# Optimization experiments

Hardware: AMD Instinct MI355X
Metric: run time of the kernel (lower is better)

Reference implementation:

```python
import jax, jax.numpy as jnp
import numpy as np

TEMPERATURE = 0.07
EPS = 1e-8  # torch cosine_similarity clamps the norm product at eps


def setup_inputs() -> dict:
    key = jax.random.key(0)
    k1, k2 = jax.random.split(key)
    B, D = 8192, 256
    u = jax.random.normal(k1, (B, D), dtype=jnp.float32)
    v = jax.random.normal(k2, (B, D), dtype=jnp.float32)
    return {"u": u, "v": v}


def _cos_sim_matrix(a, b):
    # pairwise cosine similarity: (a . b) / max(|a||b|, eps)
    dots = a @ b.T                                   # [B, B]
    an = jnp.linalg.norm(a, axis=-1)                 # [B]
    bn = jnp.linalg.norm(b, axis=-1)                 # [B]
    denom = jnp.maximum(an[:, None] * bn[None, :], EPS)
    return dots / denom


def reference(u, v):
    B = u.shape[0]
    sim_uv = _cos_sim_matrix(u, v) / TEMPERATURE     # [B, B]
    sim_uu = _cos_sim_matrix(u, u) / TEMPERATURE     # [B, B]
    eye = jnp.eye(B, dtype=bool)
    pos_loss = jnp.diagonal(sim_uv)                  # [B]
    neg_inf = jnp.array(-jnp.inf, dtype=sim_uv.dtype)
    # off-diagonal entries of both matrices, concatenated per row (2B-2 valid each)
    negative_sim = jnp.concatenate(
        [jnp.where(eye, neg_inf, sim_uv), jnp.where(eye, neg_inf, sim_uu)], axis=1
    )                                                # [B, 2B]
    neg_loss = jax.nn.logsumexp(negative_sim, axis=-1)  # [B]
    return (-pos_loss + neg_loss).mean()
```

## Files before the change

kernel.cpp:

```cpp
#include <hip/hip_runtime.h>
#include <hip/hip_bf16.h>
#include <stdint.h>

#define NB 8192
#define ND 256
#define NW 16384
#define BM 128
#define BN 128
#define NSTRIP 4
#define STRIPW 4096
#define NTILES (STRIPW / BN)
#define SQRT_INVT 3.7796447f

typedef __bf16 bf16x8 __attribute__((ext_vector_type(8)));
typedef float floatx4 __attribute__((ext_vector_type(4)));

__device__ __forceinline__ void gload_lds16(const void* g, void* l) {
    __builtin_amdgcn_global_load_lds(
        (const __attribute__((address_space(1))) unsigned int*)g,
        (__attribute__((address_space(3))) unsigned int*)l,
        16, 0, 0);
}

__global__ __launch_bounds__(512) void prep_kernel(
    const float* __restrict__ u, const float* __restrict__ v,
    __hip_bfloat16* __restrict__ W)
{
    const int t    = threadIdx.x;
    const int row  = blockIdx.x * 8 + (t >> 6);
    const int lane = t & 63;
    const float* src = (row < NB) ? (v + (size_t)row * ND)
                                  : (u + (size_t)(row - NB) * ND);
    float4 x = ((const float4*)src)[lane];
    float ss = x.x * x.x + x.y * x.y + x.z * x.z + x.w * x.w;
#pragma unroll
    for (int off = 1; off < 64; off <<= 1) ss += __shfl_xor(ss, off, 64);
    const float sc = rsqrtf(ss) * SQRT_INVT;
    ushort4 o;
    __hip_bfloat16 h;
    h = __float2bfloat16(x.x * sc); o.x = *(const unsigned short*)&h;
    h = __float2bfloat16(x.y * sc); o.y = *(const unsigned short*)&h;
    h = __float2bfloat16(x.z * sc); o.z = *(const unsigned short*)&h;
    h = __float2bfloat16(x.w * sc); o.w = *(const unsigned short*)&h;
    ((ushort4*)(W + (size_t)row * ND))[lane] = o;
}

__global__ __launch_bounds__(512, 2) void dcl_main(
    const __hip_bfloat16* __restrict__ W,
    float* __restrict__ partial,
    float* __restrict__ pos)
{
    const int b  = blockIdx.x;
    const int s  = (b >> 1) & 3;
    const int rt = ((b >> 3) << 1) | (b & 1);
    const int rb = rt * BM;

    const __hip_bfloat16* A = W + (size_t)NB * ND;

    __shared__ __align__(16) char lds[131072];

    const int tid  = threadIdx.x;
    const int wave = tid >> 6;
    const int lane = tid & 63;
    const int wm   = wave >> 2;
    const int wn   = wave & 3;
    const int quad = lane >> 4;
    const int tcol = lane & 15;

    {
        const int cb0 = s * STRIPW;
#pragma unroll
        for (int i = 0; i < 8; i++) {
            int o = i * 8192 + wave * 1024 + lane * 16;
            int r = o >> 9;
            int c = (o >> 4) & 31;
            int cg = (c ^ (r & 15)) * 8;
            gload_lds16(A + (size_t)(rb + r) * ND + cg,
                        lds + i * 8192 + wave * 1024);
            gload_lds16(W + (size_t)(cb0 + r) * ND + cg,
                        lds + 65536 + i * 8192 + wave * 1024);
        }
    }
    __syncthreads();

    bf16x8 af[4][8];
#pragma unroll
    for (int mt = 0; mt < 4; mt++) {
        int r = wm * 64 + mt * 16 + tcol;
#pragma unroll
        for (int ks = 0; ks < 8; ks++) {
            int c = (ks * 4 + quad) ^ (r & 15);
            af[mt][ks] = *(const bf16x8*)(lds + r * 512 + (c << 4));
        }
    }
    __syncthreads();

    float rsum[4][4];
#pragma unroll
    for (int mt = 0; mt < 4; mt++)
#pragma unroll
        for (int reg = 0; reg < 4; reg++) rsum[mt][reg] = 0.f;

    for (int ct = 0; ct < NTILES; ct++) {
        char* curB = (ct & 1) ? lds : (lds + 65536);
        if (ct + 1 < NTILES) {
            char* nxt = ((ct + 1) & 1) ? lds : (lds + 65536);
            const int cbn = s * STRIPW + (ct + 1) * BN;
#pragma unroll
            for (int i = 0; i < 8; i++) {
                int o = i * 8192 + wave * 1024 + lane * 16;
                int r = o >> 9;
                int c = (o >> 4) & 31;
                int cg = (c ^ (r & 15)) * 8;
                gload_lds16(W + (size_t)(cbn + r) * ND + cg,
                            nxt + i * 8192 + wave * 1024);
            }
        }
        const int cb = s * STRIPW + ct * BN;

        floatx4 acc[4][2];
#pragma unroll
        for (int mt = 0; mt < 4; mt++)
#pragma unroll
            for (int nt = 0; nt < 2; nt++) acc[mt][nt] = (floatx4){0.f, 0.f, 0.f, 0.f};

#pragma unroll
        for (int ks = 0; ks < 8; ks++) {
            bf16x8 bfr[2];
#pragma unroll
            for (int nt = 0; nt < 2; nt++) {
                int r = wn * 32 + nt * 16 + tcol;
                int c = (ks * 4 + quad) ^ (r & 15);
                bfr[nt] = *(const bf16x8*)(curB + r * 512 + (c << 4));
            }
#pragma unroll
            for (int mt = 0; mt < 4; mt++)
#pragma unroll
                for (int nt = 0; nt < 2; nt++)
                    acc[mt][nt] = __builtin_amdgcn_mfma_f32_16x16x32_bf16(
                        af[mt][ks], bfr[nt], acc[mt][nt], 0, 0, 0);
        }

        if (cb != rb && cb != rb + NB) {
#pragma unroll
            for (int mt = 0; mt < 4; mt++)
#pragma unroll
                for (int nt = 0; nt < 2; nt++)
#pragma unroll
                    for (int reg = 0; reg < 4; reg++)
                        rsum[mt][reg] += __expf(acc[mt][nt][reg]);
        } else {
            const bool isuv = (cb == rb);
#pragma unroll
            for (int mt = 0; mt < 4; mt++)
#pragma unroll
                for (int nt = 0; nt < 2; nt++) {
                    const int gcol = cb + wn * 32 + nt * 16 + tcol;
#pragma unroll
                    for (int reg = 0; reg < 4; reg++) {
                        const int grow = rb + wm * 64 + mt * 16 + quad * 4 + reg;
                        float sc = acc[mt][nt][reg];
                        bool diag = (gcol == grow + (isuv ? 0 : NB));
                        if (isuv && diag) pos[grow] = sc;
                        rsum[mt][reg] += diag ? 0.f : __expf(sc);
                    }
                }
        }
        __syncthreads();
    }

#pragma unroll
    for (int mt = 0; mt < 4; mt++)
#pragma unroll
        for (int reg = 0; reg < 4; reg++) {
            float vsum = rsum[mt][reg];
            vsum += __shfl_xor(vsum, 1, 64);
            vsum += __shfl_xor(vsum, 2, 64);
            vsum += __shfl_xor(vsum, 4, 64);
            vsum += __shfl_xor(vsum, 8, 64);
            if (tcol == 0) {
                int lrow = wm * 64 + mt * 16 + quad * 4 + reg;
                ((float*)lds)[wn * 128 + lrow] = vsum;
            }
        }
    __syncthreads();
    if (tid < BM) {
        const float* lf = (const float*)lds;
        float t = lf[tid] + lf[128 + tid] + lf[256 + tid] + lf[384 + tid];
        partial[(size_t)s * NB + rb + tid] = t;
    }
}

__global__ __launch_bounds__(1024) void finalize_kernel(
    const float* __restrict__ partial, const float* __restrict__ pos,
    float* __restrict__ out)
{
    const int t = threadIdx.x;
    float s = 0.f;
    for (int i = t; i < NB; i += 1024) {
        float tot = partial[i] + partial[NB + i] + partial[2 * NB + i]
                  + partial[3 * NB + i];
        s += logf(tot) - pos[i];
    }
#pragma unroll
    for (int off = 32; off > 0; off >>= 1) s += __shfl_down(s, off, 64);
    __shared__ float wsum[16];
    if ((t & 63) == 0) wsum[t >> 6] = s;
    __syncthreads();
    if (t == 0) {
        float tot = 0.f;
#pragma unroll
        for (int i = 0; i < 16; i++) tot += wsum[i];
        out[0] = tot / (float)NB;
    }
}

extern "C" void kernel_launch(void* const* d_in, const int* in_sizes, int n_in,
                              void* d_out, int out_size, void* d_ws, size_t ws_size,
                              hipStream_t stream) {
    const float* u = (const float*)d_in[0];
    const float* v = (const float*)d_in[1];
    float* out = (float*)d_out;

    char* ws = (char*)d_ws;
    __hip_bfloat16* W = (__hip_bfloat16*)ws;
    float* partial = (float*)(ws + (size_t)NW * ND * sizeof(__hip_bfloat16));
    float* pos     = partial + NSTRIP * NB;

    prep_kernel<<<NW / 8, 512, 0, stream>>>(u, v, W);
    dcl_main<<<256, 512, 0, stream>>>(W, partial, pos);
    finalize_kernel<<<1, 1024, 0, stream>>>(partial, pos, out);
}
```

Measured before the change: 135.3 us.

## Give each wave private double-buffered B tiles and software-pipeline exp with MFMA

Each wave now loads its own 16-row slice of the column tile into a private LDS double buffer. This removes the block-wide __syncthreads in the main loop and synchronises only with per-wave vmcnt waits. The loop is software-pipelined so the exp epilogue of one tile overlaps the MFMA of the next, with s_setprio raising priority around MFMA issue. Diagonal entries are handled by subtracting their exp after the fact rather than branching per tile. This trades smaller tiles (BN 64) and some exp-subtraction precision risk for less synchronisation and better overlap of the exp and MFMA work.

```diff
diff --git a/kernel.cpp b/kernel.cpp
--- a/kernel.cpp
+++ b/kernel.cpp
@@ -6,7 +6,7 @@
 #define ND 256
 #define NW 16384
 #define BM 128
-#define BN 128
+#define BN 64
 #define NSTRIP 4
 #define STRIPW 4096
 #define NTILES (STRIPW / BN)
@@ -66,20 +66,16 @@
     const int wn   = wave & 3;
     const int quad = lane >> 4;
     const int tcol = lane & 15;
-
-    {
-        const int cb0 = s * STRIPW;
-#pragma unroll
-        for (int i = 0; i < 8; i++) {
-            int o = i * 8192 + wave * 1024 + lane * 16;
-            int r = o >> 9;
-            int c = (o >> 4) & 31;
-            int cg = (c ^ (r & 15)) * 8;
-            gload_lds16(A + (size_t)(rb + r) * ND + cg,
-                        lds + i * 8192 + wave * 1024);
-            gload_lds16(W + (size_t)(cb0 + r) * ND + cg,
-                        lds + 65536 + i * 8192 + wave * 1024);
-        }
+    const int cc   = lane & 31;
+    const int rh   = lane >> 5;
+
+#pragma unroll
+    for (int i = 0; i < 8; i++) {
+        int o = i * 8192 + wave * 1024 + lane * 16;
+        int r = o >> 9;
+        int c = (o >> 4) & 31;
+        int cg = (c ^ (r & 15)) * 8;
+        gload_lds16(A + (size_t)(rb + r) * ND + cg, lds + i * 8192 + wave * 1024);
     }
     __syncthreads();
 
@@ -95,79 +91,106 @@
     }
     __syncthreads();
 
+    char* const wbuf  = lds + wave * 16384;
+    const int   sbase = s * STRIPW;
+
+    const bool isuv = (s < 2);
+    int dp = rb + wm * 64 + (isuv ? 0 : NB);
+    if ((dp >> 12) != s) dp = 0x40000000;
+
     float rsum[4][4];
 #pragma unroll
     for (int mt = 0; mt < 4; mt++)
 #pragma unroll
-        for (int reg = 0; reg < 4; reg++) rsum[mt][reg] = 0.f;
-
-    for (int ct = 0; ct < NTILES; ct++) {
-        char* curB = (ct & 1) ? lds : (lds + 65536);
-        if (ct + 1 < NTILES) {
-            char* nxt = ((ct + 1) & 1) ? lds : (lds + 65536);
-            const int cbn = s * STRIPW + (ct + 1) * BN;
-#pragma unroll
-            for (int i = 0; i < 8; i++) {
-                int o = i * 8192 + wave * 1024 + lane * 16;
-                int r = o >> 9;
-                int c = (o >> 4) & 31;
-                int cg = (c ^ (r & 15)) * 8;
-                gload_lds16(W + (size_t)(cbn + r) * ND + cg,
-                            nxt + i * 8192 + wave * 1024);
-            }
-        }
-        const int cb = s * STRIPW + ct * BN;
-
-        floatx4 acc[4][2];
-#pragma unroll
-        for (int mt = 0; mt < 4; mt++)
-#pragma unroll
-            for (int nt = 0; nt < 2; nt++) acc[mt][nt] = (floatx4){0.f, 0.f, 0.f, 0.f};
-
-#pragma unroll
-        for (int ks = 0; ks < 8; ks++) {
-            bf16x8 bfr[2];
-#pragma unroll
-            for (int nt = 0; nt < 2; nt++) {
-                int r = wn * 32 + nt * 16 + tcol;
-                int c = (ks * 4 + quad) ^ (r & 15);
-                bfr[nt] = *(const bf16x8*)(curB + r * 512 + (c << 4));
-            }
-#pragma unroll
-            for (int mt = 0; mt < 4; mt++)
-#pragma unroll
-                for (int nt = 0; nt < 2; nt++)
-                    acc[mt][nt] = __builtin_amdgcn_mfma_f32_16x16x32_bf16(
-                        af[mt][ks], bfr[nt], acc[mt][nt], 0, 0, 0);
-        }
-
-        if (cb != rb && cb != rb + NB) {
-#pragma unroll
-            for (int mt = 0; mt < 4; mt++)
-#pragma unroll
-                for (int nt = 0; nt < 2; nt++)
-#pragma unroll
-                    for (int reg = 0; reg < 4; reg++)
-                        rsum[mt][reg] += __expf(acc[mt][nt][reg]);
-        } else {
-            const bool isuv = (cb == rb);
-#pragma unroll
-            for (int mt = 0; mt < 4; mt++)
-#pragma unroll
-                for (int nt = 0; nt < 2; nt++) {
-                    const int gcol = cb + wn * 32 + nt * 16 + tcol;
-#pragma unroll
-                    for (int reg = 0; reg < 4; reg++) {
-                        const int grow = rb + wm * 64 + mt * 16 + quad * 4 + reg;
-                        float sc = acc[mt][nt][reg];
-                        bool diag = (gcol == grow + (isuv ? 0 : NB));
-                        if (isuv && diag) pos[grow] = sc;
-                        rsum[mt][reg] += diag ? 0.f : __expf(sc);
-                    }
-                }
-        }
-        __syncthreads();
-    }
+        for (int rg = 0; rg < 4; rg++) rsum[mt][rg] = 0.f;
+
+#define STAGE(t, half) do {                                                  \
+    const int rowb_ = sbase + (t) * BN + wn * 16;                            \
+    char* dst_ = wbuf + (half) * 8192;                                       \
+    _Pragma("unroll")                                                        \
+    for (int i_ = 0; i_ < 8; i_++) {                                         \
+        int r_ = 2 * i_ + rh;                                                \
+        gload_lds16(W + (size_t)(rowb_ + r_) * ND + ((cc ^ r_) << 3),        \
+                    dst_ + i_ * 1024);                                       \
+    }                                                                        \
+} while (0)
+
+#define EPI_CLEAN(accP) do {                                                 \
+    _Pragma("unroll")                                                        \
+    for (int mt_ = 0; mt_ < 4; mt_++)                                        \
+        _Pragma("unroll")                                                    \
+        for (int rg_ = 0; rg_ < 4; rg_++)                                    \
+            rsum[mt_][rg_] += __expf(accP[mt_][rg_]);                        \
+} while (0)
+
+#define FIXUP(accP, cbP) do {                                                \
+    if ((cbP) == dp) {                                                       \
+        _Pragma("unroll")                                                    \
+        for (int mt_ = 0; mt_ < 4; mt_++)                                    \
+            _Pragma("unroll")                                                \
+            for (int rg_ = 0; rg_ < 4; rg_++) {                              \
+                int rl_ = mt_ * 16 + quad * 4 + rg_;                         \
+                bool sel_ = (rl_ == wn * 16 + tcol);                         \
+                float sc_ = accP[mt_][rg_];                                  \
+                if (isuv && sel_) pos[rb + wm * 64 + rl_] = sc_;             \
+                if (sel_) rsum[mt_][rg_] -= __expf(sc_);                     \
+            }                                                                \
+    }                                                                        \
+} while (0)
+
+#define COMPUTE(acc, bufp) do {                                              \
+    _Pragma("unroll")                                                        \
+    for (int mt_ = 0; mt_ < 4; mt_++) acc[mt_] = (floatx4){0.f,0.f,0.f,0.f}; \
+    __builtin_amdgcn_s_setprio(1);                                           \
+    _Pragma("unroll")                                                        \
+    for (int ks_ = 0; ks_ < 8; ks_++) {                                      \
+        bf16x8 bb_ = *(const bf16x8*)((bufp) + tcol * 512 +                  \
+                                      ((((ks_ * 4) + quad) ^ tcol) << 4));   \
+        _Pragma("unroll")                                                    \
+        for (int mt_ = 0; mt_ < 4; mt_++)                                    \
+            acc[mt_] = __builtin_amdgcn_mfma_f32_16x16x32_bf16(              \
+                af[mt_][ks_], bb_, acc[mt_], 0, 0, 0);                       \
+    }                                                                        \
+    __builtin_amdgcn_s_setprio(0);                                           \
+} while (0)
+
+    floatx4 accA[4], accB[4];
+#pragma unroll
+    for (int mt = 0; mt < 4; mt++)
+        accB[mt] = (floatx4){-1e38f, -1e38f, -1e38f, -1e38f};
+    int cbA = -1, cbB = -1;
+
+    STAGE(0, 0);
+
+#pragma unroll 1
+    for (int t2 = 0; t2 < NTILES; t2 += 2) {
+        asm volatile("s_waitcnt vmcnt(0)" ::: "memory");
+        STAGE(t2 + 1, 1);
+        __builtin_amdgcn_sched_barrier(0);
+        EPI_CLEAN(accB);
+        COMPUTE(accA, wbuf);
+        __builtin_amdgcn_sched_barrier(0);
+        FIXUP(accB, cbB);
+        cbA = sbase + t2 * BN;
+
+        asm volatile("s_waitcnt vmcnt(0)" ::: "memory");
+        if (t2 + 2 < NTILES) STAGE(t2 + 2, 0);
+        __builtin_amdgcn_sched_barrier(0);
+        EPI_CLEAN(accA);
+        COMPUTE(accB, wbuf + 8192);
+        __builtin_amdgcn_sched_barrier(0);
+        FIXUP(accA, cbA);
+        cbB = sbase + (t2 + 1) * BN;
+    }
+    EPI_CLEAN(accB);
+    FIXUP(accB, cbB);
+
+#undef STAGE
+#undef EPI_CLEAN
+#undef FIXUP
+#undef COMPUTE
+
+    __syncthreads();
 
 #pragma unroll
     for (int mt = 0; mt < 4; mt++)
```

Result: no change. 137.4 us (+1.5%).

## Split column range into eight shards with 64-wide tiles and higher occupancy

Applied to the files above, without the earlier changes.

The work is split into 8 column shards of 2048 (512 blocks) instead of 4 strips (256 blocks). Tiles are now 64 columns wide, so LDS use halves to 64KB and launch bounds allow 4 blocks per CU. A fragments are now loaded directly from global into registers instead of staged through LDS. The loop also adds sched_barrier/setprio hints and a simpler diagonal test. The aim is more parallelism and overlap to hide latency, at the cost of smaller tiles with less B reuse per tile and more partial sums for the finalize kernel to combine.

```diff
diff --git a/kernel.cpp b/kernel.cpp
--- a/kernel.cpp
+++ b/kernel.cpp
@@ -6,10 +6,10 @@
 #define ND 256
 #define NW 16384
 #define BM 128
-#define BN 128
-#define NSTRIP 4
-#define STRIPW 4096
-#define NTILES (STRIPW / BN)
+#define BN 64
+#define NSH 8
+#define SHW 2048
+#define NTILES (SHW / BN)
 #define SQRT_INVT 3.7796447f
 
 typedef __bf16 bf16x8 __attribute__((ext_vector_type(8)));
@@ -45,19 +45,21 @@
     ((ushort4*)(W + (size_t)row * ND))[lane] = o;
 }
 
-__global__ __launch_bounds__(512, 2) void dcl_main(
+__global__ __launch_bounds__(512, 4) void dcl_main(
     const __hip_bfloat16* __restrict__ W,
     float* __restrict__ partial,
     float* __restrict__ pos)
 {
     const int b  = blockIdx.x;
-    const int s  = (b >> 1) & 3;
-    const int rt = ((b >> 3) << 1) | (b & 1);
+    const int x  = b & 7;
+    const int j  = b >> 3;
+    const int sh = ((x & 3) << 1) | (j & 1);
+    const int rt = (j >> 1) | ((x >> 2) << 5);
     const int rb = rt * BM;
 
     const __hip_bfloat16* A = W + (size_t)NB * ND;
 
-    __shared__ __align__(16) char lds[131072];
+    __shared__ __align__(16) char lds[65536];
 
     const int tid  = threadIdx.x;
     const int wave = tid >> 6;
@@ -67,107 +69,90 @@
     const int quad = lane >> 4;
     const int tcol = lane & 15;
 
-    {
-        const int cb0 = s * STRIPW;
-#pragma unroll
-        for (int i = 0; i < 8; i++) {
-            int o = i * 8192 + wave * 1024 + lane * 16;
-            int r = o >> 9;
-            int c = (o >> 4) & 31;
-            int cg = (c ^ (r & 15)) * 8;
-            gload_lds16(A + (size_t)(rb + r) * ND + cg,
-                        lds + i * 8192 + wave * 1024);
-            gload_lds16(W + (size_t)(cb0 + r) * ND + cg,
-                        lds + 65536 + i * 8192 + wave * 1024);
+#define STAGE(t, slot) do {                                                  \
+    const int cbW_ = sh * SHW + (t) * BN;                                    \
+    char* dst_ = lds + (slot) * 32768;                                       \
+    _Pragma("unroll")                                                        \
+    for (int i_ = 0; i_ < 4; i_++) {                                         \
+        int o_ = i_ * 8192 + wave * 1024 + lane * 16;                        \
+        int r_ = o_ >> 9;                                 \
+        int c_ = (o_ >> 4) & 31;                              \
+        int cg_ = (c_ ^ (r_ & 15)) * 8;               \
+        gload_lds16(W + (size_t)(cbW_ + r_) * ND + cg_,                      \
+                    dst_ + i_ * 8192 + wave * 1024);                         \
+    }                                                                        \
+} while (0)
+
+    STAGE(0, 0);
+
+    bf16x8 af[4][8];
+#pragma unroll
+    for (int mt = 0; mt < 4; mt++) {
+        const __hip_bfloat16* ar =
+            A + (size_t)(rb + wm * 64 + mt * 16 + tcol) * ND + quad * 8;
+#pragma unroll
+        for (int ks = 0; ks < 8; ks++)
+            af[mt][ks] = *(const bf16x8*)(ar + ks * 32);
+    }
+
+    const bool isuv = (sh < 4);
+    int dp = rb + wm * 64 + (isuv ? 0 : NB);
+    if ((dp >> 11) != sh) dp = 0x40000000;
+
+    float rsum[4][4];
+#pragma unroll
+    for (int mt = 0; mt < 4; mt++)
+#pragma unroll
+        for (int rg = 0; rg < 4; rg++) rsum[mt][rg] = 0.f;
+
+#pragma unroll 1
+    for (int t = 0; t < NTILES; t++) {
+        __syncthreads();
+        if (t + 1 < NTILES) STAGE(t + 1, (t + 1) & 1);
+        __builtin_amdgcn_sched_barrier(0);
+
+        const char* curB = lds + (t & 1) * 32768;
+        floatx4 acc[4];
+#pragma unroll
+        for (int mt = 0; mt < 4; mt++) acc[mt] = (floatx4){0.f, 0.f, 0.f, 0.f};
+
+        __builtin_amdgcn_s_setprio(1);
+#pragma unroll
+        for (int ks = 0; ks < 8; ks++) {
+            bf16x8 bb = *(const bf16x8*)(curB + (wn * 16 + tcol) * 512 +
+                                         ((((ks * 4) + quad) ^ tcol) << 4));
+#pragma unroll
+            for (int mt = 0; mt < 4; mt++)
+                acc[mt] = __builtin_amdgcn_mfma_f32_16x16x32_bf16(
+                    af[mt][ks], bb, acc[mt], 0, 0, 0);
         }
-    }
-    __syncthreads();
-
-    bf16x8 af[4][8];
-#pragma unroll
-    for (int mt = 0; mt < 4; mt++) {
-        int r = wm * 64 + mt * 16 + tcol;
-#pragma unroll
-        for (int ks = 0; ks < 8; ks++) {
-            int c = (ks * 4 + quad) ^ (r & 15);
-            af[mt][ks] = *(const bf16x8*)(lds + r * 512 + (c << 4));
-        }
-    }
-    __syncthreads();
-
-    float rsum[4][4];
-#pragma unroll
-    for (int mt = 0; mt < 4; mt++)
-#pragma unroll
-        for (int reg = 0; reg < 4; reg++) rsum[mt][reg] = 0.f;
-
-    for (int ct = 0; ct < NTILES; ct++) {
-        char* curB = (ct & 1) ? lds : (lds + 65536);
-        if (ct + 1 < NTILES) {
-            char* nxt = ((ct + 1) & 1) ? lds : (lds + 65536);
-            const int cbn = s * STRIPW + (ct + 1) * BN;
-#pragma unroll
-            for (int i = 0; i < 8; i++) {
-                int o = i * 8192 + wave * 1024 + lane * 16;
-                int r = o >> 9;
-                int c = (o >> 4) & 31;
-                int cg = (c ^ (r & 15)) * 8;
-                gload_lds16(W + (size_t)(cbn + r) * ND + cg,
-                            nxt + i * 8192 + wave * 1024);
-            }
-        }
-        const int cb = s * STRIPW + ct * BN;
-
-        floatx4 acc[4][2];
-#pragma unroll
-        for (int mt = 0; mt < 4; mt++)
-#pragma unroll
-            for (int nt = 0; nt < 2; nt++) acc[mt][nt] = (floatx4){0.f, 0.f, 0.f, 0.f};
-
-#pragma unroll
-        for (int ks = 0; ks < 8; ks++) {
-            bf16x8 bfr[2];
-#pragma unroll
-            for (int nt = 0; nt < 2; nt++) {
-                int r = wn * 32 + nt * 16 + tcol;
-                int c = (ks * 4 + quad) ^ (r & 15);
-                bfr[nt] = *(const bf16x8*)(curB + r * 512 + (c << 4));
-            }
+        __builtin_amdgcn_s_setprio(0);
+        __builtin_amdgcn_sched_barrier(0);
+
+        const int cb = sh * SHW + t * BN;
+        if (cb != dp) {
 #pragma unroll
             for (int mt = 0; mt < 4; mt++)
 #pragma unroll
-                for (int nt = 0; nt < 2; nt++)
-                    acc[mt][nt] = __builtin_amdgcn_mfma_f32_16x16x32_bf16(
-                        af[mt][ks], bfr[nt], acc[mt][nt], 0, 0, 0);
-        }
-
-        if (cb != rb && cb != rb + NB) {
+                for (int rg = 0; rg < 4; rg++)
+                    rsum[mt][rg] += __expf(acc[mt][rg]);
+        } else {
 #pragma unroll
             for (int mt = 0; mt < 4; mt++)
 #pragma unroll
-                for (int nt = 0; nt < 2; nt++)
-#pragma unroll
-                    for (int reg = 0; reg < 4; reg++)
-                        rsum[mt][reg] += __expf(acc[mt][nt][reg]);
-        } else {
-            const bool isuv = (cb == rb);
-#pragma unroll
-            for (int mt = 0; mt < 4; mt++)
-#pragma unroll
-                for (int nt = 0; nt < 2; nt++) {
-                    const int gcol = cb + wn * 32 + nt * 16 + tcol;
-#pragma unroll
-                    for (int reg = 0; reg < 4; reg++) {
-                        const int grow = rb + wm * 64 + mt * 16 + quad * 4 + reg;
-                        float sc = acc[mt][nt][reg];
-                        bool diag = (gcol == grow + (isuv ? 0 : NB));
-                        if (isuv && diag) pos[grow] = sc;
-                        rsum[mt][reg] += diag ? 0.f : __expf(sc);
-                    }
+                for (int rg = 0; rg < 4; rg++) {
+                    int rl = mt * 16 + quad * 4 + rg;
+                    bool sel = (rl == wn * 16 + tcol);
+                    float sc = acc[mt][rg];
+                    if (isuv && sel) pos[rb + wm * 64 + rl] = sc;
+                    rsum[mt][rg] += sel ? 0.f : __expf(sc);
                 }
         }
-        __syncthreads();
-    }
+    }
+
+#undef STAGE
+
+    __syncthreads();
 
 #pragma unroll
     for (int mt = 0; mt < 4; mt++)
@@ -187,7 +172,7 @@
     if (tid < BM) {
         const float* lf = (const float*)lds;
         float t = lf[tid] + lf[128 + tid] + lf[256 + tid] + lf[384 + tid];
-        partial[(size_t)s * NB + rb + tid] = t;
+        partial[(size_t)sh * NB + rb + tid] = t;
     }
 }
 
@@ -198,8 +183,9 @@
     const int t = threadIdx.x;
     float s = 0.f;
     for (int i = t; i < NB; i += 1024) {
-        float tot = partial[i] + partial[NB + i] + partial[2 * NB + i]
-                  + partial[3 * NB + i];
+        float tot = 0.f;
+#pragma unroll
+        for (int k = 0; k < NSH; k++) tot += partial[(size_t)k * NB + i];
         s += logf(tot) - pos[i];
     }
 #pragma unroll
@@ -225,9 +211,9 @@
     char* ws = (char*)d_ws;
     __hip_bfloat16* W = (__hip_bfloat16*)ws;
     float* partial = (float*)(ws + (size_t)NW * ND * sizeof(__hip_bfloat16));
-    float* pos     = partial + NSTRIP * NB;
+    float* pos     = partial + NSH * NB;
 
     prep_kernel<<<NW / 8, 512, 0, stream>>>(u, v, W);
-    dcl_main<<<256, 512, 0, stream>>>(W, partial, pos);
+    dcl_main<<<512, 512, 0, stream>>>(W, partial, pos);
     finalize_kernel<<<1, 1024, 0, stream>>>(partial, pos, out);
 }
```

Measured after the change: 415.6 us. +207.1%, slower.
